# Optimization experiments

Hardware: AMD Instinct MI355X
Metric: run time of the kernel (lower is better)

Reference implementation:

```python
import jax, jax.numpy as jnp
import numpy as np

NUM_TOKENS = 16384
MODEL_DIM = 4096
MAX_EXPERTS = 128
INITIAL_EXPERTS = 64
THRESHOLD = 0.5  # rm_threshold


def setup_inputs() -> dict:
    key = jax.random.key(0)
    k1, k2 = jax.random.split(key)
    x = jax.random.normal(k1, (NUM_TOKENS, MODEL_DIM), dtype=jnp.float32)
    # Linear(model_dim, max_expert_num, bias=False).weight -> [E_max, D]
    wg_weight = jax.random.normal(k2, (MAX_EXPERTS, MODEL_DIM), dtype=jnp.float32) * (1.0 / np.sqrt(MODEL_DIM))
    # experts_mask: first `INITIAL_EXPERTS` active
    experts_mask = (jnp.arange(MAX_EXPERTS) < INITIAL_EXPERTS).astype(jnp.float32)
    return {"x": x, "wg_weight": wg_weight, "experts_mask": experts_mask}


def reference(x, wg_weight, experts_mask):
    # gate logits: [N, E_max]
    scores = jnp.einsum("nd,ed->ne", x, wg_weight)
    # mask inactive experts
    scores = jnp.where(experts_mask[None, :] == 0, jnp.float32(-1e9), scores)
    # fp32 softmax + epsilon (matches F.softmax(..., dtype=float32) + 1e-14)
    scores = jax.nn.softmax(scores.astype(jnp.float32), axis=-1) + 1e-14
    # sort descending along expert dim
    sorted_scores = -jnp.sort(-scores, axis=-1)
    cum_scores = jnp.cumsum(sorted_scores, axis=-1)
    # adaptive top-k: experts needed to accumulate THRESHOLD routing mass
    mask = (cum_scores - sorted_scores) < THRESHOLD
    top_k = mask.sum(axis=-1).astype(jnp.int32)
    active_experts = experts_mask.sum().astype(jnp.int32)
    top_k = jnp.minimum(top_k, active_experts)
    return scores.astype(x.dtype), top_k
```

## Files before the change

### kernel.cpp

```cpp
#include <hip/hip_runtime.h>
#include <hip/hip_bf16.h>
#include <stdint.h>

#define NTOK 16384
#define DDIM 4096
#define NEXP 128
#define BM 32
#define BK 64
#define BKP 72

typedef __attribute__((ext_vector_type(8))) short short8;
typedef __attribute__((ext_vector_type(4))) float f32x4;

__device__ __forceinline__ void split_bf16(float f, uint32_t& h, uint32_t& l) {
    uint32_t u = __float_as_uint(f);
    h = (u + 0x7FFFu + ((u >> 16) & 1u)) >> 16;
    float r = f - __uint_as_float(h << 16);
    uint32_t v = __float_as_uint(r);
    l = (v + 0x7FFFu + ((v >> 16) & 1u)) >> 16;
}

__global__ void prep_w(const float* __restrict__ w,
                       uint16_t* __restrict__ whi, uint16_t* __restrict__ wlo) {
    int i = (blockIdx.x * blockDim.x + threadIdx.x) * 4;
    float4 f = *(const float4*)(w + i);
    uint32_t h0, h1, h2, h3, l0, l1, l2, l3;
    split_bf16(f.x, h0, l0);
    split_bf16(f.y, h1, l1);
    split_bf16(f.z, h2, l2);
    split_bf16(f.w, h3, l3);
    uint2 hv = make_uint2(h0 | (h1 << 16), h2 | (h3 << 16));
    uint2 lv = make_uint2(l0 | (l1 << 16), l2 | (l3 << 16));
    *(uint2*)(whi + i) = hv;
    *(uint2*)(wlo + i) = lv;
}

__global__ __launch_bounds__(256, 2) void gemm_logits(
    const float* __restrict__ x,
    const uint16_t* __restrict__ whi, const uint16_t* __restrict__ wlo,
    float* __restrict__ S)
{
    __shared__ uint16_t sAh[BM * BKP], sAl[BM * BKP];
    __shared__ uint16_t sBh[NEXP * BKP], sBl[NEXP * BKP];

    const int tid  = threadIdx.x;
    const int lane = tid & 63;
    const int wave = tid >> 6;
    const int m0   = blockIdx.x * BM;

    const int am  = tid >> 3;
    const int akc = tid & 7;
    const float* xp = x + (size_t)(m0 + am) * DDIM + akc * 8;

    f32x4 acc[2][2];
    #pragma unroll
    for (int mt = 0; mt < 2; ++mt)
        #pragma unroll
        for (int nt = 0; nt < 2; ++nt)
            acc[mt][nt] = (f32x4){0.f, 0.f, 0.f, 0.f};

    const int q = lane >> 4;
    const int c = lane & 15;

    for (int k0 = 0; k0 < DDIM; k0 += BK) {
        float4 fa = *(const float4*)(xp + k0);
        float4 fb = *(const float4*)(xp + k0 + 4);
        uint32_t h[8], l[8];
        split_bf16(fa.x, h[0], l[0]); split_bf16(fa.y, h[1], l[1]);
        split_bf16(fa.z, h[2], l[2]); split_bf16(fa.w, h[3], l[3]);
        split_bf16(fb.x, h[4], l[4]); split_bf16(fb.y, h[5], l[5]);
        split_bf16(fb.z, h[6], l[6]); split_bf16(fb.w, h[7], l[7]);
        uint4 hv = make_uint4(h[0] | (h[1] << 16), h[2] | (h[3] << 16),
                              h[4] | (h[5] << 16), h[6] | (h[7] << 16));
        uint4 lv = make_uint4(l[0] | (l[1] << 16), l[2] | (l[3] << 16),
                              l[4] | (l[5] << 16), l[6] | (l[7] << 16));
        *(uint4*)&sAh[am * BKP + akc * 8] = hv;
        *(uint4*)&sAl[am * BKP + akc * 8] = lv;

        #pragma unroll
        for (int i = 0; i < 4; ++i) {
            int ch = tid + i * 256;
            int n = ch >> 3, kc = ch & 7;
            const size_t go = (size_t)n * DDIM + k0 + kc * 8;
            uint4 bh = *(const uint4*)(whi + go);
            uint4 bl = *(const uint4*)(wlo + go);
            *(uint4*)&sBh[n * BKP + kc * 8] = bh;
            *(uint4*)&sBl[n * BKP + kc * 8] = bl;
        }
        __syncthreads();

        #pragma unroll
        for (int ks = 0; ks < 2; ++ks) {
            const int kb = ks * 32 + q * 8;
            short8 ah[2], alo[2], bh[2], blo[2];
            #pragma unroll
            for (int mt = 0; mt < 2; ++mt) {
                const int ro = (mt * 16 + c) * BKP + kb;
                ah[mt]  = *(const short8*)&sAh[ro];
                alo[mt] = *(const short8*)&sAl[ro];
            }
            #pragma unroll
            for (int nt = 0; nt < 2; ++nt) {
                const int ro = (wave * 32 + nt * 16 + c) * BKP + kb;
                bh[nt]  = *(const short8*)&sBh[ro];
                blo[nt] = *(const short8*)&sBl[ro];
            }
            #pragma unroll
            for (int mt = 0; mt < 2; ++mt)
                #pragma unroll
                for (int nt = 0; nt < 2; ++nt) {
                    acc[mt][nt] = __builtin_amdgcn_mfma_f32_16x16x32_bf16(alo[mt], bh[nt],  acc[mt][nt], 0, 0, 0);
                    acc[mt][nt] = __builtin_amdgcn_mfma_f32_16x16x32_bf16(ah[mt],  blo[nt], acc[mt][nt], 0, 0, 0);
                    acc[mt][nt] = __builtin_amdgcn_mfma_f32_16x16x32_bf16(ah[mt],  bh[nt],  acc[mt][nt], 0, 0, 0);
                }
        }
        __syncthreads();
    }

    #pragma unroll
    for (int mt = 0; mt < 2; ++mt)
        #pragma unroll
        for (int nt = 0; nt < 2; ++nt) {
            const int e = wave * 32 + nt * 16 + c;
            #pragma unroll
            for (int r = 0; r < 4; ++r) {
                const int tok = m0 + mt * 16 + q * 4 + r;
                S[(size_t)tok * NEXP + e] = acc[mt][nt][r];
            }
        }
}

__global__ __launch_bounds__(256) void postproc(
    float* __restrict__ S, const float* __restrict__ mask,
    float* __restrict__ topk_out)
{
    const int lane = threadIdx.x & 63;
    const int wave = threadIdx.x >> 6;
    const int t = blockIdx.x * 4 + wave;
    float* row = S + (size_t)t * NEXP;

    float s0 = row[lane], s1 = row[lane + 64];
    float mk0 = mask[lane], mk1 = mask[lane + 64];
    const bool a0 = (mk0 != 0.f), a1 = (mk1 != 0.f);

    float mx = fmaxf(a0 ? s0 : -3.0e38f, a1 ? s1 : -3.0e38f);
    #pragma unroll
    for (int off = 32; off; off >>= 1) mx = fmaxf(mx, __shfl_xor(mx, off));

    float p0 = a0 ? __expf(s0 - mx) : 0.f;
    float p1 = a1 ? __expf(s1 - mx) : 0.f;
    float sum = p0 + p1;
    #pragma unroll
    for (int off = 32; off; off >>= 1) sum += __shfl_xor(sum, off);

    const float inv = 1.0f / sum;
    const float sc0 = p0 * inv + 1e-14f;
    const float sc1 = p1 * inv + 1e-14f;
    row[lane]      = sc0;
    row[lane + 64] = sc1;

    const int active = __popcll(__ballot(a0)) + __popcll(__ballot(a1));

    float v0 = sc0, v1 = sc1;
    float cum = 0.f;
    int k = 0;
    while (cum < 0.5f && k < NEXP) {
        float mv = fmaxf(v0, v1);
        #pragma unroll
        for (int off = 32; off; off >>= 1) mv = fmaxf(mv, __shfl_xor(mv, off));
        cum += mv;
        ++k;
        unsigned long long b = __ballot(v0 == mv || v1 == mv);
        int first = __ffsll(b) - 1;
        if (lane == first) {
            if (v0 == mv) v0 = -1.f; else v1 = -1.f;
        }
    }
    int topk = k < active ? k : active;
    if (lane == 0) topk_out[t] = (float)topk;
}

extern "C" void kernel_launch(void* const* d_in, const int* in_sizes, int n_in,
                              void* d_out, int out_size, void* d_ws, size_t ws_size,
                              hipStream_t stream) {
    (void)in_sizes; (void)n_in; (void)out_size; (void)ws_size;
    const float* x    = (const float*)d_in[0];
    const float* w    = (const float*)d_in[1];
    const float* mask = (const float*)d_in[2];

    float* S    = (float*)d_out;
    float* topk = S + (size_t)NTOK * NEXP;

    uint16_t* whi = (uint16_t*)d_ws;
    uint16_t* wlo = whi + (size_t)NEXP * DDIM;

    hipLaunchKernelGGL(prep_w, dim3((NEXP * DDIM) / (256 * 4)), dim3(256), 0, stream,
                       w, whi, wlo);
    hipLaunchKernelGGL(gemm_logits, dim3(NTOK / BM), dim3(256), 0, stream,
                       x, whi, wlo, S);
    hipLaunchKernelGGL(postproc, dim3(NTOK / 4), dim3(256), 0, stream,
                       S, mask, topk);
}
```

Before: 418.7 us.

## Fuse softmax/top-k into GEMM epilogue and use direct global-to-LDS weight loads

Merges the postprocessing kernel into the GEMM by staging logits in shared memory and running softmax and adaptive top-k per token in the epilogue, which removes the logits round-trip through global memory and one launch. Weight tiles are now loaded with global_load_lds into an XOR-swizzled, unpadded LDS layout instead of going through registers. The next x tile is prefetched into registers before the MFMA loop. In exchange, the extra 16KB LDS logits buffer may lower occupancy, and the serial top-k loop now sits inside the GEMM blocks.

Result: slower. 433.4 us (+3.5%).

```diff
diff --git a/kernel.cpp b/kernel.cpp
--- a/kernel.cpp
+++ b/kernel.cpp
@@ -18,6 +18,12 @@
     float r = f - __uint_as_float(h << 16);
     uint32_t v = __float_as_uint(r);
     l = (v + 0x7FFFu + ((v >> 16) & 1u)) >> 16;
+}
+
+__device__ __forceinline__ void gld_lds16(const void* g, void* l) {
+    __builtin_amdgcn_global_load_lds(
+        (const __attribute__((address_space(1))) void*)g,
+        (__attribute__((address_space(3))) void*)l, 16, 0, 0);
 }
 
 __global__ void prep_w(const float* __restrict__ w,
@@ -29,29 +35,35 @@
     split_bf16(f.y, h1, l1);
     split_bf16(f.z, h2, l2);
     split_bf16(f.w, h3, l3);
-    uint2 hv = make_uint2(h0 | (h1 << 16), h2 | (h3 << 16));
-    uint2 lv = make_uint2(l0 | (l1 << 16), l2 | (l3 << 16));
-    *(uint2*)(whi + i) = hv;
-    *(uint2*)(wlo + i) = lv;
-}
-
-__global__ __launch_bounds__(256, 2) void gemm_logits(
+    *(uint2*)(whi + i) = make_uint2(h0 | (h1 << 16), h2 | (h3 << 16));
+    *(uint2*)(wlo + i) = make_uint2(l0 | (l1 << 16), l2 | (l3 << 16));
+}
+
+__global__ __launch_bounds__(256, 2) void gate_fused(
     const float* __restrict__ x,
     const uint16_t* __restrict__ whi, const uint16_t* __restrict__ wlo,
-    float* __restrict__ S)
+    const float* __restrict__ mask,
+    float* __restrict__ S, float* __restrict__ topk_out)
 {
     __shared__ uint16_t sAh[BM * BKP], sAl[BM * BKP];
-    __shared__ uint16_t sBh[NEXP * BKP], sBl[NEXP * BKP];
+    __shared__ uint16_t sBh[NEXP * BK], sBl[NEXP * BK];
+    __shared__ float    L[BM][NEXP];
 
     const int tid  = threadIdx.x;
     const int lane = tid & 63;
     const int wave = tid >> 6;
     const int m0   = blockIdx.x * BM;
 
+    const float mk0 = mask[lane];
+    const float mk1 = mask[lane + 64];
+
     const int am  = tid >> 3;
     const int akc = tid & 7;
     const float* xp = x + (size_t)(m0 + am) * DDIM + akc * 8;
 
+    float4 fa = *(const float4*)(xp);
+    float4 fb = *(const float4*)(xp + 4);
+
     f32x4 acc[2][2];
     #pragma unroll
     for (int mt = 0; mt < 2; ++mt)
@@ -62,36 +74,46 @@
     const int q = lane >> 4;
     const int c = lane & 15;
 
+    int bn[4], bkc[4];
+    #pragma unroll
+    for (int j = 0; j < 4; ++j) {
+        const int p = (wave * 4 + j) * 64 + lane;
+        bn[j]  = p >> 3;
+        bkc[j] = (p & 7) ^ (bn[j] & 7);
+    }
+
     for (int k0 = 0; k0 < DDIM; k0 += BK) {
-        float4 fa = *(const float4*)(xp + k0);
-        float4 fb = *(const float4*)(xp + k0 + 4);
         uint32_t h[8], l[8];
         split_bf16(fa.x, h[0], l[0]); split_bf16(fa.y, h[1], l[1]);
         split_bf16(fa.z, h[2], l[2]); split_bf16(fa.w, h[3], l[3]);
         split_bf16(fb.x, h[4], l[4]); split_bf16(fb.y, h[5], l[5]);
         split_bf16(fb.z, h[6], l[6]); split_bf16(fb.w, h[7], l[7]);
-        uint4 hv = make_uint4(h[0] | (h[1] << 16), h[2] | (h[3] << 16),
-                              h[4] | (h[5] << 16), h[6] | (h[7] << 16));
-        uint4 lv = make_uint4(l[0] | (l[1] << 16), l[2] | (l[3] << 16),
-                              l[4] | (l[5] << 16), l[6] | (l[7] << 16));
-        *(uint4*)&sAh[am * BKP + akc * 8] = hv;
-        *(uint4*)&sAl[am * BKP + akc * 8] = lv;
-
-        #pragma unroll
-        for (int i = 0; i < 4; ++i) {
-            int ch = tid + i * 256;
-            int n = ch >> 3, kc = ch & 7;
-            const size_t go = (size_t)n * DDIM + k0 + kc * 8;
-            uint4 bh = *(const uint4*)(whi + go);
-            uint4 bl = *(const uint4*)(wlo + go);
-            *(uint4*)&sBh[n * BKP + kc * 8] = bh;
-            *(uint4*)&sBl[n * BKP + kc * 8] = bl;
+        *(uint4*)&sAh[am * BKP + akc * 8] =
+            make_uint4(h[0] | (h[1] << 16), h[2] | (h[3] << 16),
+                       h[4] | (h[5] << 16), h[6] | (h[7] << 16));
+        *(uint4*)&sAl[am * BKP + akc * 8] =
+            make_uint4(l[0] | (l[1] << 16), l[2] | (l[3] << 16),
+                       l[4] | (l[5] << 16), l[6] | (l[7] << 16));
+
+        #pragma unroll
+        for (int j = 0; j < 4; ++j) {
+            const size_t go = (size_t)bn[j] * DDIM + k0 + bkc[j] * 8;
+            const int lb = (wave * 4 + j) * 512;
+            gld_lds16(whi + go, sBh + lb);
+            gld_lds16(wlo + go, sBl + lb);
         }
         __syncthreads();
 
+        {
+            const int kn = (k0 + BK < DDIM) ? (k0 + BK) : 0;
+            fa = *(const float4*)(xp + kn);
+            fb = *(const float4*)(xp + kn + 4);
+        }
+
         #pragma unroll
         for (int ks = 0; ks < 2; ++ks) {
-            const int kb = ks * 32 + q * 8;
+            const int kb  = ks * 32 + q * 8;
+            const int kb8 = ks * 4 + q;
             short8 ah[2], alo[2], bh[2], blo[2];
             #pragma unroll
             for (int mt = 0; mt < 2; ++mt) {
@@ -101,9 +123,10 @@
             }
             #pragma unroll
             for (int nt = 0; nt < 2; ++nt) {
-                const int ro = (wave * 32 + nt * 16 + c) * BKP + kb;
-                bh[nt]  = *(const short8*)&sBh[ro];
-                blo[nt] = *(const short8*)&sBl[ro];
+                const int ne = wave * 32 + nt * 16 + c;
+                const int ch = ne * 8 + (kb8 ^ (ne & 7));
+                bh[nt]  = *(const short8*)&sBh[ch * 8];
+                blo[nt] = *(const short8*)&sBl[ch * 8];
             }
             #pragma unroll
             for (int mt = 0; mt < 2; ++mt)
@@ -123,61 +146,53 @@
         for (int nt = 0; nt < 2; ++nt) {
             const int e = wave * 32 + nt * 16 + c;
             #pragma unroll
-            for (int r = 0; r < 4; ++r) {
-                const int tok = m0 + mt * 16 + q * 4 + r;
-                S[(size_t)tok * NEXP + e] = acc[mt][nt][r];
+            for (int r = 0; r < 4; ++r)
+                L[mt * 16 + q * 4 + r][e] = acc[mt][nt][r];
+        }
+    __syncthreads();
+
+    const bool a0 = (mk0 != 0.f), a1 = (mk1 != 0.f);
+    const int active = __popcll(__ballot(a0)) + __popcll(__ballot(a1));
+
+    for (int i = 0; i < 8; ++i) {
+        const int lt  = wave * 8 + i;
+        const int tok = m0 + lt;
+        float s0 = L[lt][lane], s1 = L[lt][lane + 64];
+
+        float mx = fmaxf(a0 ? s0 : -3.0e38f, a1 ? s1 : -3.0e38f);
+        #pragma unroll
+        for (int off = 32; off; off >>= 1) mx = fmaxf(mx, __shfl_xor(mx, off));
+
+        float p0 = a0 ? __expf(s0 - mx) : 0.f;
+        float p1 = a1 ? __expf(s1 - mx) : 0.f;
+        float sum = p0 + p1;
+        #pragma unroll
+        for (int off = 32; off; off >>= 1) sum += __shfl_xor(sum, off);
+
+        const float inv = 1.0f / sum;
+        const float sc0 = p0 * inv + 1e-14f;
+        const float sc1 = p1 * inv + 1e-14f;
+        S[(size_t)tok * NEXP + lane]      = sc0;
+        S[(size_t)tok * NEXP + lane + 64] = sc1;
+
+        float v0 = sc0, v1 = sc1;
+        float cum = 0.f;
+        int k = 0;
+        while (cum < 0.5f && k < NEXP) {
+            float mv = fmaxf(v0, v1);
+            #pragma unroll
+            for (int off = 32; off; off >>= 1) mv = fmaxf(mv, __shfl_xor(mv, off));
+            cum += mv;
+            ++k;
+            unsigned long long b = __ballot(v0 == mv || v1 == mv);
+            int first = __ffsll(b) - 1;
+            if (lane == first) {
+                if (v0 == mv) v0 = -1.f; else v1 = -1.f;
             }
         }
-}
-
-__global__ __launch_bounds__(256) void postproc(
-    float* __restrict__ S, const float* __restrict__ mask,
-    float* __restrict__ topk_out)
-{
-    const int lane = threadIdx.x & 63;
-    const int wave = threadIdx.x >> 6;
-    const int t = blockIdx.x * 4 + wave;
-    float* row = S + (size_t)t * NEXP;
-
-    float s0 = row[lane], s1 = row[lane + 64];
-    float mk0 = mask[lane], mk1 = mask[lane + 64];
-    const bool a0 = (mk0 != 0.f), a1 = (mk1 != 0.f);
-
-    float mx = fmaxf(a0 ? s0 : -3.0e38f, a1 ? s1 : -3.0e38f);
-    #pragma unroll
-    for (int off = 32; off; off >>= 1) mx = fmaxf(mx, __shfl_xor(mx, off));
-
-    float p0 = a0 ? __expf(s0 - mx) : 0.f;
-    float p1 = a1 ? __expf(s1 - mx) : 0.f;
-    float sum = p0 + p1;
-    #pragma unroll
-    for (int off = 32; off; off >>= 1) sum += __shfl_xor(sum, off);
-
-    const float inv = 1.0f / sum;
-    const float sc0 = p0 * inv + 1e-14f;
-    const float sc1 = p1 * inv + 1e-14f;
-    row[lane]      = sc0;
-    row[lane + 64] = sc1;
-
-    const int active = __popcll(__ballot(a0)) + __popcll(__ballot(a1));
-
-    float v0 = sc0, v1 = sc1;
-    float cum = 0.f;
-    int k = 0;
-    while (cum < 0.5f && k < NEXP) {
-        float mv = fmaxf(v0, v1);
-        #pragma unroll
-        for (int off = 32; off; off >>= 1) mv = fmaxf(mv, __shfl_xor(mv, off));
-        cum += mv;
-        ++k;
-        unsigned long long b = __ballot(v0 == mv || v1 == mv);
-        int first = __ffsll(b) - 1;
-        if (lane == first) {
-            if (v0 == mv) v0 = -1.f; else v1 = -1.f;
-        }
+        int topk = k < active ? k : active;
+        if (lane == 0) topk_out[tok] = (float)topk;
     }
-    int topk = k < active ? k : active;
-    if (lane == 0) topk_out[t] = (float)topk;
 }
 
 extern "C" void kernel_launch(void* const* d_in, const int* in_sizes, int n_in,
@@ -196,8 +211,6 @@
 
     hipLaunchKernelGGL(prep_w, dim3((NEXP * DDIM) / (256 * 4)), dim3(256), 0, stream,
                        w, whi, wlo);
-    hipLaunchKernelGGL(gemm_logits, dim3(NTOK / BM), dim3(256), 0, stream,
-                       x, whi, wlo, S);
-    hipLaunchKernelGGL(postproc, dim3(NTOK / 4), dim3(256), 0, stream,
-                       S, mask, topk);
-}
+    hipLaunchKernelGGL(gate_fused, dim3(NTOK / BM), dim3(256), 0, stream,
+                       x, whi, wlo, mask, S, topk);
+}
```
